# Optimization experiments

Hardware: AMD Instinct MI355X
Metric: run time of the kernel (lower is better)

## Reference

```python
import math
import jax, jax.numpy as jnp
import numpy as np

B, TQ, TK = 16, 2048, 1024
D_DEC, D_ENC, D_ATT = 256, 256, 128
WINDOW_SIZE = 3


def setup_inputs() -> dict:
    key = jax.random.key(0)
    ks = jax.random.split(key, 11)
    s = 0.02
    return {
        "query": jax.random.normal(ks[0], (B, TQ, D_DEC), jnp.float32),
        "keys": jax.random.normal(ks[1], (B, TK, D_ENC), jnp.float32),
        "values": jax.random.normal(ks[2], (B, TK, D_ENC), jnp.float32),
        "Wq": jax.random.normal(ks[3], (D_ATT, D_DEC), jnp.float32) * s,
        "bq": jax.random.normal(ks[4], (D_ATT,), jnp.float32) * s,
        "Wk": jax.random.normal(ks[5], (D_ATT, D_ENC), jnp.float32) * s,
        "bk": jax.random.normal(ks[6], (D_ATT,), jnp.float32) * s,
        "Wv": jax.random.normal(ks[7], (D_ATT, D_ENC), jnp.float32) * s,
        "bv": jax.random.normal(ks[8], (D_ATT,), jnp.float32) * s,
        "Wo": jax.random.normal(ks[9], (D_DEC, D_ATT), jnp.float32) * s,
        "bo": jax.random.normal(ks[10], (D_DEC,), jnp.float32) * s,
        "prev_max_attention_idx": 100,
    }


def reference(query, keys, values, Wq, bq, Wk, bk, Wv, bv, Wo, bo,
              prev_max_attention_idx):
    residual = query
    q = query @ Wq.T + bq            # [B, Tq, A]
    k = keys @ Wk.T + bk             # [B, Tk, A]
    v = values @ Wv.T + bv           # [B, Tk, A]
    scores = jnp.einsum('bqa,bka->bqk', q, k)  # [B, Tq, Tk]
    Tk = scores.shape[-1]
    col = jnp.arange(Tk)
    # mask [:prev] if prev > 0, and [prev + window :] if in range
    masked = (col < prev_max_attention_idx) | (col >= prev_max_attention_idx + WINDOW_SIZE)
    scores = jnp.where(masked[None, None, :], -jnp.inf, scores)
    attn = jax.nn.softmax(scores, axis=-1)
    attn_scores = attn
    # dropout_prob = 0.0 -> identity
    ctx = jnp.einsum('bqk,bka->bqa', attn, v)
    s = v.shape[1]
    ctx = ctx * (s * math.sqrt(1.0 / s))  # == sqrt(Tk)
    out = (ctx @ Wo.T + bo + residual) * math.sqrt(0.5)
    return (out, attn_scores)
```

## Files before the change

kernel.cpp:

```cpp
#include <hip/hip_runtime.h>
#include <math.h>

#define BATCH 16
#define TQL   2048
#define TKL   1024
#define DDEC  256
#define DENC  256
#define DATT  128
#define WIN   3

#define WS_KQ 0
#define WS_VO (48*DDEC)
#define WS_KB (2*48*DDEC)

#define NZBLK 2048

__global__ __launch_bounds__(256) void pre_and_zero(
    const float* __restrict__ keys, const float* __restrict__ values,
    const float* __restrict__ Wk, const float* __restrict__ bk,
    const float* __restrict__ Wv, const float* __restrict__ bv,
    const float* __restrict__ Wq, const float* __restrict__ bq,
    const float* __restrict__ Wo, const int* __restrict__ pidx,
    float* __restrict__ ws, float* __restrict__ attn)
{
    const int t = threadIdx.x;

    if (blockIdx.x >= 48) {
        const int zb = blockIdx.x - 48;
        float4* p = (float4*)attn + (size_t)zb * 4096;
        const float4 z4 = make_float4(0.0f, 0.0f, 0.0f, 0.0f);
        #pragma unroll
        for (int i = 0; i < 16; ++i) p[i * 256 + t] = z4;
        return;
    }

    const int blk = blockIdx.x;
    const int b = blk / WIN, j = blk % WIN;
    const int prev = pidx[0];
    const int col = prev + j;
    const bool valid = (col >= 0) && (col < TKL);

    __shared__ float ksh[DENC];
    __shared__ float vsh[DENC];
    __shared__ float kwsh[DATT];
    __shared__ float vwsh[DATT];

    {
        size_t base = ((size_t)b * TKL + (valid ? col : 0)) * DENC + t;
        ksh[t] = valid ? keys[base]   : 0.0f;
        vsh[t] = valid ? values[base] : 0.0f;
    }
    __syncthreads();

    if (t < DATT) {
        const float4* wrow = (const float4*)(Wk + (size_t)t * DENC);
        float acc = 0.0f;
        #pragma unroll 8
        for (int k4 = 0; k4 < DENC / 4; ++k4) {
            float4 w = wrow[k4];
            acc += w.x * ksh[k4*4+0] + w.y * ksh[k4*4+1]
                 + w.z * ksh[k4*4+2] + w.w * ksh[k4*4+3];
        }
        kwsh[t] = acc + bk[t];
    } else {
        const int c = t - DATT;
        const float4* wrow = (const float4*)(Wv + (size_t)c * DENC);
        float acc = 0.0f;
        #pragma unroll 8
        for (int k4 = 0; k4 < DENC / 4; ++k4) {
            float4 w = wrow[k4];
            acc += w.x * vsh[k4*4+0] + w.y * vsh[k4*4+1]
                 + w.z * vsh[k4*4+2] + w.w * vsh[k4*4+3];
        }
        vwsh[c] = acc + bv[c];
    }
    __syncthreads();

    float accq = 0.0f, acco = 0.0f;
    const float4* worow = (const float4*)(Wo + (size_t)t * DATT);
    #pragma unroll 4
    for (int c4 = 0; c4 < DATT / 4; ++c4) {
        float4 w = worow[c4];
        acco += w.x * vwsh[c4*4+0] + w.y * vwsh[c4*4+1]
              + w.z * vwsh[c4*4+2] + w.w * vwsh[c4*4+3];
        accq += kwsh[c4*4+0] * Wq[(size_t)(c4*4+0) * DDEC + t]
              + kwsh[c4*4+1] * Wq[(size_t)(c4*4+1) * DDEC + t]
              + kwsh[c4*4+2] * Wq[(size_t)(c4*4+2) * DDEC + t]
              + kwsh[c4*4+3] * Wq[(size_t)(c4*4+3) * DDEC + t];
    }
    ws[WS_KQ + blk * DDEC + t] = accq;
    ws[WS_VO + blk * DDEC + t] = acco;

    if (t < 64) {
        float pb = bq[t] * kwsh[t] + bq[t + 64] * kwsh[t + 64];
        #pragma unroll
        for (int off = 32; off > 0; off >>= 1) pb += __shfl_xor(pb, off, 64);
        if (t == 0) ws[WS_KB + blk] = pb;
    }
}

__device__ __forceinline__ float winval(int ww, float w0, float w1, float w2) {
    float v = (ww == 0) ? w0 : ((ww == 1) ? w1 : ((ww == 2) ? w2 : 0.0f));
    return (ww >= 0 && ww < WIN) ? v : 0.0f;
}

#define ROWS_PER_WAVE 8

__global__ __launch_bounds__(256) void attn_out(
    const float* __restrict__ query, const float* __restrict__ bo,
    const int* __restrict__ pidx, const float* __restrict__ ws,
    float* __restrict__ out, float* __restrict__ attn)
{
    const int t    = threadIdx.x;
    const int lane = t & 63;
    const int wid  = t >> 6;
    const int blk  = blockIdx.x;
    const int b    = blk >> 6;
    const int base = b * WIN;
    const int prev = pidx[0];
    const int row0 = blk * (4 * ROWS_PER_WAVE) + wid * ROWS_PER_WAVE;

    const float4* qp = (const float4*)query;
    float4 q[ROWS_PER_WAVE];
    #pragma unroll
    for (int r = 0; r < ROWS_PER_WAVE; ++r)
        q[r] = qp[(size_t)(row0 + r) * 64 + lane];

    const float4* kq4 = (const float4*)(ws + WS_KQ) + (size_t)base * 64;
    const float4* vo4 = (const float4*)(ws + WS_VO) + (size_t)base * 64;
    const float4 K0 = kq4[      lane];
    const float4 K1 = kq4[ 64 + lane];
    const float4 K2 = kq4[128 + lane];
    const float4 V0 = vo4[      lane];
    const float4 V1 = vo4[ 64 + lane];
    const float4 V2 = vo4[128 + lane];
    const float4 B4 = ((const float4*)bo)[lane];
    const float kb0 = ws[WS_KB + base + 0];
    const float kb1 = ws[WS_KB + base + 1];
    const float kb2 = ws[WS_KB + base + 2];

    int lo = prev < 0 ? 0 : prev;
    int hi = prev + (WIN - 1) > TKL - 1 ? TKL - 1 : prev + (WIN - 1);
    int f0 = -1, f1 = -1;
    if (lo <= hi) { f0 = lo >> 2; f1 = hi >> 2; }

    const bool v0 = (prev + 0 >= 0) && (prev + 0 < TKL);
    const bool v1 = (prev + 1 >= 0) && (prev + 1 < TKL);
    const bool v2 = (prev + 2 >= 0) && (prev + 2 < TKL);

    const float CTX_SCALE = 32.0f;
    const float RSQ2 = 0.70710678118654752f;
    const float NEG = -3.0e38f;

    #pragma unroll
    for (int r = 0; r < ROWS_PER_WAVE; ++r) {
        const int row = row0 + r;
        const float4 qq = q[r];

        float p0 = qq.x*K0.x + qq.y*K0.y + qq.z*K0.z + qq.w*K0.w;
        float p1 = qq.x*K1.x + qq.y*K1.y + qq.z*K1.z + qq.w*K1.w;
        float p2 = qq.x*K2.x + qq.y*K2.y + qq.z*K2.z + qq.w*K2.w;

        #pragma unroll
        for (int off = 32; off > 0; off >>= 1) {
            p0 += __shfl_xor(p0, off, 64);
            p1 += __shfl_xor(p1, off, 64);
            p2 += __shfl_xor(p2, off, 64);
        }

        float s0 = v0 ? (p0 + kb0) : NEG;
        float s1 = v1 ? (p1 + kb1) : NEG;
        float s2 = v2 ? (p2 + kb2) : NEG;

        const float m  = fmaxf(s0, fmaxf(s1, s2));
        const float e0 = v0 ? __expf(s0 - m) : 0.0f;
        const float e1 = v1 ? __expf(s1 - m) : 0.0f;
        const float e2 = v2 ? __expf(s2 - m) : 0.0f;
        const float inv = 1.0f / (e0 + e1 + e2);
        const float w0 = e0 * inv, w1 = e1 * inv, w2 = e2 * inv;

        float4 o;
        o.x = (CTX_SCALE * (w0*V0.x + w1*V1.x + w2*V2.x) + B4.x + qq.x) * RSQ2;
        o.y = (CTX_SCALE * (w0*V0.y + w1*V1.y + w2*V2.y) + B4.y + qq.y) * RSQ2;
        o.z = (CTX_SCALE * (w0*V0.z + w1*V1.z + w2*V2.z) + B4.z + qq.z) * RSQ2;
        o.w = (CTX_SCALE * (w0*V0.w + w1*V1.w + w2*V2.w) + B4.w + qq.w) * RSQ2;
        ((float4*)(out + (size_t)row * DDEC))[lane] = o;

        if (f0 >= 0 && lane == 0) {
            const int c0 = f0 * 4;
            float4 pz;
            pz.x = winval(c0 + 0 - prev, w0, w1, w2);
            pz.y = winval(c0 + 1 - prev, w0, w1, w2);
            pz.z = winval(c0 + 2 - prev, w0, w1, w2);
            pz.w = winval(c0 + 3 - prev, w0, w1, w2);
            ((float4*)(attn + (size_t)row * TKL))[f0] = pz;
        }
        if (f1 != f0 && lane == 1) {
            const int c0 = f1 * 4;
            float4 pz;
            pz.x = winval(c0 + 0 - prev, w0, w1, w2);
            pz.y = winval(c0 + 1 - prev, w0, w1, w2);
            pz.z = winval(c0 + 2 - prev, w0, w1, w2);
            pz.w = winval(c0 + 3 - prev, w0, w1, w2);
            ((float4*)(attn + (size_t)row * TKL))[f1] = pz;
        }
    }
}

extern "C" void kernel_launch(void* const* d_in, const int* in_sizes, int n_in,
                              void* d_out, int out_size, void* d_ws, size_t ws_size,
                              hipStream_t stream)
{
    const float* query  = (const float*)d_in[0];
    const float* keys   = (const float*)d_in[1];
    const float* values = (const float*)d_in[2];
    const float* Wq     = (const float*)d_in[3];
    const float* bq     = (const float*)d_in[4];
    const float* Wk     = (const float*)d_in[5];
    const float* bk     = (const float*)d_in[6];
    const float* Wv     = (const float*)d_in[7];
    const float* bv     = (const float*)d_in[8];
    const float* Wo     = (const float*)d_in[9];
    const float* bo     = (const float*)d_in[10];
    const int*   pidx   = (const int*)d_in[11];

    float* ws   = (float*)d_ws;
    float* out  = (float*)d_out;
    float* attn = out + (size_t)BATCH * TQL * DDEC;

    pre_and_zero<<<48 + NZBLK, 256, 0, stream>>>(keys, values, Wk, bk, Wv, bv,
                                                 Wq, bq, Wo, pidx, ws, attn);
    attn_out<<<BATCH * TQL / 32, 256, 0, stream>>>(query, bo, pidx, ws, out, attn);
}
```

Before: 42.42 us.

## Split into three kernels: precompute, weight compute, and fused zero-fill with window inject

The precompute stage now splits each (batch, window) pair across two blocks, one for the key/query projection and one for the value/output projection, doubling parallelism there. The output kernel uses 4 rows per wave instead of 8 and no longer writes into the attention matrix. It stores two softmax weights per row to the workspace. A third kernel zero-fills the full attention matrix and writes the window weights in the same pass, rebuilding w2 as 1-w0-w1. This avoids writing the same attention rows twice, at the cost of an extra launch and a slightly different rounding for the third weight.

```diff
diff --git a/kernel.cpp b/kernel.cpp
--- a/kernel.cpp
+++ b/kernel.cpp
@@ -12,118 +12,91 @@
 #define WS_KQ 0
 #define WS_VO (48*DDEC)
 #define WS_KB (2*48*DDEC)
-
-#define NZBLK 2048
-
-__global__ __launch_bounds__(256) void pre_and_zero(
+#define WS_W  (WS_KB + 64)
+
+__global__ __launch_bounds__(256) void precompute(
     const float* __restrict__ keys, const float* __restrict__ values,
     const float* __restrict__ Wk, const float* __restrict__ bk,
     const float* __restrict__ Wv, const float* __restrict__ bv,
     const float* __restrict__ Wq, const float* __restrict__ bq,
     const float* __restrict__ Wo, const int* __restrict__ pidx,
-    float* __restrict__ ws, float* __restrict__ attn)
-{
-    const int t = threadIdx.x;
-
-    if (blockIdx.x >= 48) {
-        const int zb = blockIdx.x - 48;
-        float4* p = (float4*)attn + (size_t)zb * 4096;
-        const float4 z4 = make_float4(0.0f, 0.0f, 0.0f, 0.0f);
-        #pragma unroll
-        for (int i = 0; i < 16; ++i) p[i * 256 + t] = z4;
-        return;
-    }
-
-    const int blk = blockIdx.x;
-    const int b = blk / WIN, j = blk % WIN;
+    float* __restrict__ ws)
+{
+    const int blk  = blockIdx.x;
+    const int pair = blk >> 1;
+    const int role = blk & 1;
+    const int b = pair / WIN, j = pair % WIN;
     const int prev = pidx[0];
     const int col = prev + j;
     const bool valid = (col >= 0) && (col < TKL);
-
-    __shared__ float ksh[DENC];
-    __shared__ float vsh[DENC];
-    __shared__ float kwsh[DATT];
-    __shared__ float vwsh[DATT];
+    const int t = threadIdx.x;
+
+    __shared__ float src[DENC];
+    __shared__ float mid[DATT];
 
     {
-        size_t base = ((size_t)b * TKL + (valid ? col : 0)) * DENC + t;
-        ksh[t] = valid ? keys[base]   : 0.0f;
-        vsh[t] = valid ? values[base] : 0.0f;
+        const float* base = role ? values : keys;
+        size_t idx = ((size_t)b * TKL + (valid ? col : 0)) * DENC + t;
+        src[t] = valid ? base[idx] : 0.0f;
     }
     __syncthreads();
 
     if (t < DATT) {
-        const float4* wrow = (const float4*)(Wk + (size_t)t * DENC);
+        const float4* wrow = (const float4*)((role ? Wv : Wk) + (size_t)t * DENC);
         float acc = 0.0f;
         #pragma unroll 8
         for (int k4 = 0; k4 < DENC / 4; ++k4) {
             float4 w = wrow[k4];
-            acc += w.x * ksh[k4*4+0] + w.y * ksh[k4*4+1]
-                 + w.z * ksh[k4*4+2] + w.w * ksh[k4*4+3];
-        }
-        kwsh[t] = acc + bk[t];
+            acc += w.x * src[k4*4+0] + w.y * src[k4*4+1]
+                 + w.z * src[k4*4+2] + w.w * src[k4*4+3];
+        }
+        mid[t] = acc + (role ? bv[t] : bk[t]);
+    }
+    __syncthreads();
+
+    if (role == 0) {
+        float accq = 0.0f;
+        #pragma unroll 4
+        for (int c = 0; c < DATT; ++c)
+            accq += mid[c] * Wq[(size_t)c * DDEC + t];
+        ws[WS_KQ + pair * DDEC + t] = accq;
+        if (t < 64) {
+            float pb = bq[t] * mid[t] + bq[t + 64] * mid[t + 64];
+            #pragma unroll
+            for (int off = 32; off > 0; off >>= 1) pb += __shfl_xor(pb, off, 64);
+            if (t == 0) ws[WS_KB + pair] = pb;
+        }
     } else {
-        const int c = t - DATT;
-        const float4* wrow = (const float4*)(Wv + (size_t)c * DENC);
-        float acc = 0.0f;
-        #pragma unroll 8
-        for (int k4 = 0; k4 < DENC / 4; ++k4) {
-            float4 w = wrow[k4];
-            acc += w.x * vsh[k4*4+0] + w.y * vsh[k4*4+1]
-                 + w.z * vsh[k4*4+2] + w.w * vsh[k4*4+3];
-        }
-        vwsh[c] = acc + bv[c];
-    }
-    __syncthreads();
-
-    float accq = 0.0f, acco = 0.0f;
-    const float4* worow = (const float4*)(Wo + (size_t)t * DATT);
-    #pragma unroll 4
-    for (int c4 = 0; c4 < DATT / 4; ++c4) {
-        float4 w = worow[c4];
-        acco += w.x * vwsh[c4*4+0] + w.y * vwsh[c4*4+1]
-              + w.z * vwsh[c4*4+2] + w.w * vwsh[c4*4+3];
-        accq += kwsh[c4*4+0] * Wq[(size_t)(c4*4+0) * DDEC + t]
-              + kwsh[c4*4+1] * Wq[(size_t)(c4*4+1) * DDEC + t]
-              + kwsh[c4*4+2] * Wq[(size_t)(c4*4+2) * DDEC + t]
-              + kwsh[c4*4+3] * Wq[(size_t)(c4*4+3) * DDEC + t];
-    }
-    ws[WS_KQ + blk * DDEC + t] = accq;
-    ws[WS_VO + blk * DDEC + t] = acco;
-
-    if (t < 64) {
-        float pb = bq[t] * kwsh[t] + bq[t + 64] * kwsh[t + 64];
-        #pragma unroll
-        for (int off = 32; off > 0; off >>= 1) pb += __shfl_xor(pb, off, 64);
-        if (t == 0) ws[WS_KB + blk] = pb;
-    }
-}
-
-__device__ __forceinline__ float winval(int ww, float w0, float w1, float w2) {
-    float v = (ww == 0) ? w0 : ((ww == 1) ? w1 : ((ww == 2) ? w2 : 0.0f));
-    return (ww >= 0 && ww < WIN) ? v : 0.0f;
-}
-
-#define ROWS_PER_WAVE 8
-
-__global__ __launch_bounds__(256) void attn_out(
+        const float4* worow = (const float4*)(Wo + (size_t)t * DATT);
+        float acco = 0.0f;
+        #pragma unroll 4
+        for (int c4 = 0; c4 < DATT / 4; ++c4) {
+            float4 w = worow[c4];
+            acco += w.x * mid[c4*4+0] + w.y * mid[c4*4+1]
+                  + w.z * mid[c4*4+2] + w.w * mid[c4*4+3];
+        }
+        ws[WS_VO + pair * DDEC + t] = acco;
+    }
+}
+
+__global__ __launch_bounds__(256) void compute_w(
     const float* __restrict__ query, const float* __restrict__ bo,
-    const int* __restrict__ pidx, const float* __restrict__ ws,
-    float* __restrict__ out, float* __restrict__ attn)
+    const int* __restrict__ pidx, float* __restrict__ ws,
+    float* __restrict__ out)
 {
     const int t    = threadIdx.x;
     const int lane = t & 63;
     const int wid  = t >> 6;
     const int blk  = blockIdx.x;
-    const int b    = blk >> 6;
+    const int b    = blk >> 7;
     const int base = b * WIN;
     const int prev = pidx[0];
-    const int row0 = blk * (4 * ROWS_PER_WAVE) + wid * ROWS_PER_WAVE;
+    const int row0 = blk * 16 + wid * 4;
 
     const float4* qp = (const float4*)query;
-    float4 q[ROWS_PER_WAVE];
+    float4 q[4];
     #pragma unroll
-    for (int r = 0; r < ROWS_PER_WAVE; ++r)
+    for (int r = 0; r < 4; ++r)
         q[r] = qp[(size_t)(row0 + r) * 64 + lane];
 
     const float4* kq4 = (const float4*)(ws + WS_KQ) + (size_t)base * 64;
@@ -139,11 +112,6 @@
     const float kb1 = ws[WS_KB + base + 1];
     const float kb2 = ws[WS_KB + base + 2];
 
-    int lo = prev < 0 ? 0 : prev;
-    int hi = prev + (WIN - 1) > TKL - 1 ? TKL - 1 : prev + (WIN - 1);
-    int f0 = -1, f1 = -1;
-    if (lo <= hi) { f0 = lo >> 2; f1 = hi >> 2; }
-
     const bool v0 = (prev + 0 >= 0) && (prev + 0 < TKL);
     const bool v1 = (prev + 1 >= 0) && (prev + 1 < TKL);
     const bool v2 = (prev + 2 >= 0) && (prev + 2 < TKL);
@@ -152,8 +120,10 @@
     const float RSQ2 = 0.70710678118654752f;
     const float NEG = -3.0e38f;
 
+    float2* wout = (float2*)(ws + WS_W);
+
     #pragma unroll
-    for (int r = 0; r < ROWS_PER_WAVE; ++r) {
+    for (int r = 0; r < 4; ++r) {
         const int row = row0 + r;
         const float4 qq = q[r];
 
@@ -186,24 +156,50 @@
         o.w = (CTX_SCALE * (w0*V0.w + w1*V1.w + w2*V2.w) + B4.w + qq.w) * RSQ2;
         ((float4*)(out + (size_t)row * DDEC))[lane] = o;
 
-        if (f0 >= 0 && lane == 0) {
-            const int c0 = f0 * 4;
-            float4 pz;
-            pz.x = winval(c0 + 0 - prev, w0, w1, w2);
-            pz.y = winval(c0 + 1 - prev, w0, w1, w2);
-            pz.z = winval(c0 + 2 - prev, w0, w1, w2);
-            pz.w = winval(c0 + 3 - prev, w0, w1, w2);
-            ((float4*)(attn + (size_t)row * TKL))[f0] = pz;
-        }
-        if (f1 != f0 && lane == 1) {
-            const int c0 = f1 * 4;
-            float4 pz;
-            pz.x = winval(c0 + 0 - prev, w0, w1, w2);
-            pz.y = winval(c0 + 1 - prev, w0, w1, w2);
-            pz.z = winval(c0 + 2 - prev, w0, w1, w2);
-            pz.w = winval(c0 + 3 - prev, w0, w1, w2);
-            ((float4*)(attn + (size_t)row * TKL))[f1] = pz;
-        }
+        if (lane == 0) wout[row] = make_float2(w0, w1);
+    }
+}
+
+__device__ __forceinline__ float winval2(int ww, float w0, float w1, float w2) {
+    float v = (ww == 0) ? w0 : ((ww == 1) ? w1 : ((ww == 2) ? w2 : 0.0f));
+    return (ww >= 0 && ww < WIN) ? v : 0.0f;
+}
+
+__global__ __launch_bounds__(256) void fill_inject(
+    const int* __restrict__ pidx, const float* __restrict__ ws,
+    float* __restrict__ attn)
+{
+    const int t    = threadIdx.x;
+    const int blk  = blockIdx.x;
+    const int row0 = blk * 16;
+    const int prev = pidx[0];
+
+    int lo = prev < 0 ? 0 : prev;
+    int hi = prev + (WIN - 1) > TKL - 1 ? TKL - 1 : prev + (WIN - 1);
+    int f0 = -1, f1 = -1;
+    if (lo <= hi) { f0 = lo >> 2; f1 = hi >> 2; }
+
+    __shared__ float2 wsh[16];
+    if (t < 16) wsh[t] = ((const float2*)(ws + WS_W))[row0 + t];
+    __syncthreads();
+
+    float4* dst = (float4*)attn + (size_t)row0 * 256;
+    const float4 z4 = make_float4(0.0f, 0.0f, 0.0f, 0.0f);
+    const bool special = (t == f0) || (t == f1);
+    const int c0 = t * 4;
+
+    #pragma unroll
+    for (int r = 0; r < 16; ++r) {
+        float4 val = z4;
+        if (special) {
+            const float w0 = wsh[r].x, w1 = wsh[r].y;
+            const float w2 = 1.0f - w0 - w1;
+            val.x = winval2(c0 + 0 - prev, w0, w1, w2);
+            val.y = winval2(c0 + 1 - prev, w0, w1, w2);
+            val.z = winval2(c0 + 2 - prev, w0, w1, w2);
+            val.w = winval2(c0 + 3 - prev, w0, w1, w2);
+        }
+        dst[r * 256 + t] = val;
     }
 }
 
@@ -228,7 +224,8 @@
     float* out  = (float*)d_out;
     float* attn = out + (size_t)BATCH * TQL * DDEC;
 
-    pre_and_zero<<<48 + NZBLK, 256, 0, stream>>>(keys, values, Wk, bk, Wv, bv,
-                                                 Wq, bq, Wo, pidx, ws, attn);
-    attn_out<<<BATCH * TQL / 32, 256, 0, stream>>>(query, bo, pidx, ws, out, attn);
-}
+    precompute<<<96, 256, 0, stream>>>(keys, values, Wk, bk, Wv, bv,
+                                       Wq, bq, Wo, pidx, ws);
+    compute_w<<<2048, 256, 0, stream>>>(query, bo, pidx, ws, out);
+    fill_inject<<<2048, 256, 0, stream>>>(pidx, ws, attn);
+}
```

After: 54.78 us. 29.2% more time.
